# Kernel tuning notes

Measured on AMD Instinct MI355X. Metric: run time of the kernel, lower is better.

The kernel has to match this reference:

```python
import jax, jax.numpy as jnp
import numpy as np
from jax import lax

B, T, F0 = 16, 1024, 128
L_CNN, L_RNN, D = 3, 3, 512
NF = F0 // 2  # 64, freq dim after stride-2 conv
EPS = 1e-5


def conv2d(x, w, b, stride, pad):
    # x: [B,C,H,W], w: [O,I,kh,kw]
    y = lax.conv_general_dilated(x, w, (stride, stride), [(pad, pad), (pad, pad)],
                                 dimension_numbers=('NCHW', 'OIHW', 'NCHW'))
    return y + b[None, :, None, None]


def ln_last(x, g, b):
    m = x.mean(-1, keepdims=True)
    v = ((x - m) ** 2).mean(-1, keepdims=True)
    return (x - m) * lax.rsqrt(v + EPS) * g + b


def ln_feats(x, g, b):
    # LayerNorm over freq axis (axis 2) of [B,C,F,T] (== transpose(2,3); LN; transpose back)
    m = x.mean(2, keepdims=True)
    v = ((x - m) ** 2).mean(2, keepdims=True)
    return (x - m) * lax.rsqrt(v + EPS) * g[None, None, :, None] + b[None, None, :, None]


def sru_dir(u, x_res, v, b, reverse):
    # u: [T,B,3,D] (candidate, f-pre, r-pre); x_res: [T,B,D] highway input; v,b: [2,D]
    u0 = u[:, :, 0]
    fp = u[:, :, 1] + b[0]
    rp = u[:, :, 2] + b[1]

    def step(c, inp):
        u0t, fpt, rpt, xrt = inp
        f = jax.nn.sigmoid(fpt + v[0] * c)
        r = jax.nn.sigmoid(rpt + v[1] * c)
        c = f * c + (1.0 - f) * u0t
        h = r * jnp.tanh(c) + (1.0 - r) * xrt
        return c, h

    c0 = jnp.zeros(u0.shape[1:], u.dtype)
    _, h = lax.scan(step, c0, (u0, fp, rp, x_res), reverse=reverse)
    return h  # [T,B,D]


def _forward(x, cnn_w, cnn_b, res_w1, res_b1, res_w2, res_b2,
             res_ln1_g, res_ln1_b, res_ln2_g, res_ln2_b,
             proj_w, sru_w, sru_v, sru_b, sru_ln_g, sru_ln_b,
             cls_ln_g, cls_ln_b, cls_w1, cls_b1, cls_w2, cls_b2):
    # stem conv: [B,1,128,1024] -> [B,32,64,512]
    x = conv2d(x, cnn_w, cnn_b, 2, 1)
    # residual CNN blocks (dropout = identity in eval)
    for i in range(L_CNN):
        res = x
        h = jax.nn.relu(ln_feats(x, res_ln1_g[i], res_ln1_b[i]))
        h = conv2d(h, res_w1[i], res_b1[i], 1, 1)
        h = jax.nn.relu(ln_feats(h, res_ln2_g[i], res_ln2_b[i]))
        h = conv2d(h, res_w2[i], res_b2[i], 1, 1)
        x = h + res
    # flatten channels x freq, time-major: [T', B, 32*NF]
    b_, c_, f_, t_ = x.shape
    x = x.reshape(b_, c_ * f_, t_).transpose(2, 0, 1)
    # proj_input_to_hidden_first: 2048 -> 2*D
    x = jnp.einsum('tbi,ih->tbh', x, proj_w)
    # bidirectional SRU layers
    for l in range(L_RNN):
        xl = ln_last(x, sru_ln_g[l], sru_ln_b[l])
        # u: [T,B,dir,gate,D]
        u = jnp.einsum('tbi,idkh->tbdkh', xl, sru_w[l])
        h_f = sru_dir(u[:, :, 0], x[..., :D], sru_v[l, 0], sru_b[l, 0], False)
        h_b = sru_dir(u[:, :, 1], x[..., D:], sru_v[l, 1], sru_b[l, 1], True)
        x = jnp.concatenate([h_f, h_b], axis=-1)
    # classifier: [B, T', 2D] -> [B, T', n_vocab+1]
    x = x.transpose(1, 0, 2)
    x = ln_last(x, cls_ln_g, cls_ln_b)
    x = jax.nn.relu(jnp.einsum('bth,hd->btd', x, cls_w1) + cls_b1)
    x = jnp.einsum('btd,dv->btv', x, cls_w2) + cls_b2
    return x


def setup_inputs() -> dict:
    key = jax.random.key(0)
    ks = iter(jax.random.split(key, 40))

    def rn(shape, s=0.05):
        return jax.random.normal(next(ks), shape, jnp.float32) * s

    return dict(
        x=jax.random.normal(next(ks), (B, 1, F0, T), jnp.float32),
        cnn_w=rn((32, 1, 3, 3)), cnn_b=jnp.zeros(32, jnp.float32),
        res_w1=rn((L_CNN, 32, 32, 3, 3)), res_b1=jnp.zeros((L_CNN, 32), jnp.float32),
        res_w2=rn((L_CNN, 32, 32, 3, 3)), res_b2=jnp.zeros((L_CNN, 32), jnp.float32),
        res_ln1_g=jnp.ones((L_CNN, NF), jnp.float32), res_ln1_b=jnp.zeros((L_CNN, NF), jnp.float32),
        res_ln2_g=jnp.ones((L_CNN, NF), jnp.float32), res_ln2_b=jnp.zeros((L_CNN, NF), jnp.float32),
        proj_w=rn((NF * 32, 2 * D), 0.02),
        sru_w=rn((L_RNN, 2 * D, 2, 3, D), 0.02),
        sru_v=rn((L_RNN, 2, 2, D), 0.1),
        sru_b=jnp.zeros((L_RNN, 2, 2, D), jnp.float32),
        sru_ln_g=jnp.ones((L_RNN, 2 * D), jnp.float32), sru_ln_b=jnp.zeros((L_RNN, 2 * D), jnp.float32),
        cls_ln_g=jnp.ones(2 * D, jnp.float32), cls_ln_b=jnp.zeros(2 * D, jnp.float32),
        cls_w1=rn((2 * D, D), 0.02), cls_b1=jnp.zeros(D, jnp.float32),
        cls_w2=rn((D, 29), 0.02), cls_b2=jnp.zeros(29, jnp.float32),
    )


def reference(x, cnn_w, cnn_b, res_w1, res_b1, res_w2, res_b2,
              res_ln1_g, res_ln1_b, res_ln2_g, res_ln2_b,
              proj_w, sru_w, sru_v, sru_b, sru_ln_g, sru_ln_b,
              cls_ln_g, cls_ln_b, cls_w1, cls_b1, cls_w2, cls_b2):
    return _forward(x, cnn_w, cnn_b, res_w1, res_b1, res_w2, res_b2,
                    res_ln1_g, res_ln1_b, res_ln2_g, res_ln2_b,
                    proj_w, sru_w, sru_v, sru_b, sru_ln_g, sru_ln_b,
                    cls_ln_g, cls_ln_b, cls_w1, cls_b1, cls_w2, cls_b2)
```

## Files before the change

kernel.cpp:

```cpp
#include <hip/hip_runtime.h>

typedef unsigned short u16;
typedef unsigned int u32;
typedef __attribute__((ext_vector_type(8))) short short8;
typedef __attribute__((ext_vector_type(4))) float floatx4;

__device__ __forceinline__ float bf2f(u16 u) {
    union { unsigned int i; float f; } v; v.i = ((unsigned int)u) << 16; return v.f;
}
__device__ __forceinline__ u16 f2bf(float f) {
    union { float f; unsigned int i; } v; v.f = f;
    unsigned int i = v.i + 0x7fffu + ((v.i >> 16) & 1u);
    return (u16)(i >> 16);
}

#define GLL(g, l) __builtin_amdgcn_global_load_lds( \
    (const __attribute__((address_space(1))) void*)(g), \
    (__attribute__((address_space(3))) void*)(l), 16, 0, 0)

#define WAITVM(n) asm volatile("s_waitcnt vmcnt(" #n ")" ::: "memory")
#define WAITLG() asm volatile("s_waitcnt lgkmcnt(0)" ::: "memory")
#define SBAR() __builtin_amdgcn_sched_barrier(0)

#define HA_BSTRIDE 1085568

__global__ __launch_bounds__(256) void sniff_k(const u16* __restrict__ x, int* __restrict__ flag) {
    __shared__ int red[4];
    int cnt = 0;
    for (int i = 0; i < 16; ++i) {
        u16 v = x[(threadIdx.x * 16 + i) * 2];
        int e = (v >> 7) & 0xFF;
        if (e >= 110 && e <= 135) cnt++;
    }
    #pragma unroll
    for (int off = 32; off; off >>= 1) cnt += __shfl_down(cnt, off);
    if ((threadIdx.x & 63) == 0) red[threadIdx.x >> 6] = cnt;
    __syncthreads();
    if (threadIdx.x == 0) {
        int tot = red[0] + red[1] + red[2] + red[3];
        *flag = (tot < 2048) ? 1 : 0;
    }
}

__device__ __forceinline__ float ldin(const void* p, size_t i, int isf32) {
    return isf32 ? ((const float*)p)[i] : bf2f(((const u16*)p)[i]);
}

struct CvtArgs {
    const void* src[19];
    int len[19];
    int off[19];
};
__global__ __launch_bounds__(256) void cvtall_k(CvtArgs a, float* __restrict__ dst,
                                                const int* __restrict__ flag) {
    int isf32 = *flag;
    int seg = blockIdx.y;
    int n = a.len[seg];
    const void* s = a.src[seg];
    float* d = dst + a.off[seg];
    for (int i = blockIdx.x * 256 + threadIdx.x; i < n; i += gridDim.x * 256)
        d[i] = ldin(s, i, isf32);
}

__global__ __launch_bounds__(256) void wtr_k(const void* __restrict__ W, int ldw, size_t wofs,
                                             u16* __restrict__ Wt, int ldt,
                                             const int* __restrict__ flag) {
    int isf32 = *flag;
    __shared__ u16 t[64][65];
    int k0 = blockIdx.x * 64, n0 = blockIdx.y * 64;
    int tid = threadIdx.x;
    #pragma unroll
    for (int i = 0; i < 16; ++i) {
        int kk = i * 4 + (tid >> 6), nn = tid & 63;
        t[kk][nn] = f2bf(ldin(W, wofs + (size_t)(k0 + kk) * ldw + n0 + nn, isf32));
    }
    __syncthreads();
    #pragma unroll
    for (int i = 0; i < 16; ++i) {
        int nn = i * 4 + (tid >> 6), kk = tid & 63;
        Wt[(size_t)(n0 + nn) * ldt + k0 + kk] = t[kk][nn];
    }
}

__global__ __launch_bounds__(256) void zero_k(float4* __restrict__ p, int n4) {
    float4 z = {0.f, 0.f, 0.f, 0.f};
    for (int i = blockIdx.x * 256 + threadIdx.x; i < n4; i += gridDim.x * 256) p[i] = z;
}
__global__ __launch_bounds__(256) void fill_k(float* __restrict__ p, int n) {
    int i = blockIdx.x * 256 + threadIdx.x;
    if (i < n) p[i] = 1.0e6f;
}

__global__ __launch_bounds__(256) void conv1_k(const void* __restrict__ x, const float* __restrict__ w,
                                               const float* __restrict__ bias, float* __restrict__ out,
                                               const int* __restrict__ flag) {
    int isf32 = *flag;
    int idx = blockIdx.x * 256 + threadIdx.x;
    int t  = idx & 511;
    int f  = (idx >> 9) & 63;
    int cg = (idx >> 15) & 7;
    int b  = idx >> 18;
    size_t xb = (size_t)b * 128 * 1024;

    float wr[4][9];
    #pragma unroll
    for (int i = 0; i < 4; ++i)
        #pragma unroll
        for (int k = 0; k < 9; ++k) wr[i][k] = w[(cg * 4 + i) * 9 + k];

    float acc[4];
    #pragma unroll
    for (int i = 0; i < 4; ++i) acc[i] = bias[cg * 4 + i];

    #pragma unroll
    for (int df = 0; df < 3; ++df) {
        int fi = 2 * f + df - 1;
        if (fi < 0 || fi >= 128) continue;
        size_t rowb = xb + (size_t)fi * 1024;
        float xv[3];
        #pragma unroll
        for (int dt = 0; dt < 3; ++dt) {
            int ti = 2 * t + dt - 1;
            float v = 0.f;
            if (ti >= 0 && ti < 1024) v = ldin(x, rowb + ti, isf32);
            xv[dt] = v;
        }
        #pragma unroll
        for (int i = 0; i < 4; ++i)
            #pragma unroll
            for (int dt = 0; dt < 3; ++dt)
                acc[i] = fmaf(wr[i][df * 3 + dt], xv[dt], acc[i]);
    }
    size_t obase = (((size_t)b * 32 + cg * 4) * 64 + f) * 512 + t;
    #pragma unroll
    for (int i = 0; i < 4; ++i) out[obase + (size_t)i * 64 * 512] = acc[i];
}

__global__ __launch_bounds__(256) void stats_k(const void* __restrict__ X, int isbf,
                                               float* __restrict__ sm, float* __restrict__ sr) {
    int idx = blockIdx.x * 256 + threadIdx.x;
    int t  = idx & 511;
    int bc = idx >> 9;
    size_t base = (size_t)bc * 64 * 512 + t;
    float s = 0.f, s2 = 0.f;
    #pragma unroll 8
    for (int f = 0; f < 64; ++f) {
        float v = isbf ? bf2f(((const u16*)X)[base + f * 512]) : ((const float*)X)[base + f * 512];
        s += v; s2 += v * v;
    }
    sm[idx] = s;
    sr[idx] = s2;
}

__global__ __launch_bounds__(256) void apply_k(const void* __restrict__ in, int isbf,
                                               const float* __restrict__ sm, const float* __restrict__ sr,
                                               const float* __restrict__ g, const float* __restrict__ be,
                                               u16* __restrict__ Ha) {
    int f = blockIdx.x;
    int b = blockIdx.y;
    float gg = g[f], bb_ = be[f];
    for (int it = 0; it < 2; ++it) {
        int t = it * 256 + threadIdx.x;
        u32 pk[16];
        #pragma unroll
        for (int cp = 0; cp < 16; ++cp) {
            u32 w = 0;
            #pragma unroll
            for (int half = 0; half < 2; ++half) {
                int ci = cp * 2 + half;
                size_t xi = (((size_t)b * 32 + ci) * 64 + f) * 512 + t;
                float xv = isbf ? bf2f(((const u16*)in)[xi]) : ((const float*)in)[xi];
                int si = (b * 32 + ci) * 512 + t;
                float s = sm[si], s2 = sr[si];
                float m = s * (1.f / 64.f);
                float var = fmaxf(s2 * (1.f / 64.f) - m * m, 0.f);
                float rs = rsqrtf(var + 1e-5f);
                float hv = fmaxf((xv - m) * rs * gg + bb_, 0.f);
                w |= ((u32)f2bf(hv)) << (half * 16);
            }
            pk[cp] = w;
        }
        u32* orow = (u32*)(Ha + (size_t)b * HA_BSTRIDE + ((size_t)(f + 1) * 514 + (t + 1)) * 32);
        #pragma unroll
        for (int q = 0; q < 16; ++q) orow[q] = pk[q];
    }
}

#define CVL 4
__global__ __launch_bounds__(256) void convm_k(const u16* __restrict__ Ha, void* __restrict__ out,
                                               const float* __restrict__ w, const float* __restrict__ bias,
                                               const float* __restrict__ res,
                                               float* __restrict__ smx, float* __restrict__ srx) {
    __shared__ __align__(16) u16 act[2][1536 * 8];
    __shared__ float ssS[4][32][17];
    __shared__ float ssQ[4][32][17];
    int F0    = blockIdx.x * 16;
    int tbase = blockIdx.y * 64;
    int b     = blockIdx.z;
    const u16* Hb = Ha + (size_t)b * HA_BSTRIDE;
    int tid  = threadIdx.x;
    int lane = tid & 63;
    int wv   = tid >> 6;
    int quad = lane >> 4;
    int r    = lane & 15;
    int hasres  = (res != nullptr);
    int dostats = (smx != nullptr);

    int ufp[6], utp[6], uq[6];
    #pragma unroll
    for (int it = 0; it < 6; ++it) {
        int u = it * 256 + tid;
        int u2 = (u < 1296) ? u : (u - 1296);
        int fp = u2 / 72;
        int rem = u2 - fp * 72;
        ufp[it] = fp; utp[it] = rem >> 2; uq[it] = rem & 3;
    }

    auto stage = [&](int tile, int bw) {
        int t00 = tbase + tile * 16;
        #pragma unroll
        for (int it = 0; it < 6; ++it) {
            int u = it * 256 + tid;
            GLL(Hb + ((size_t)(F0 + ufp[it]) * 514 + (t00 + utp[it])) * 32 + uq[it] * 8,
                &act[bw][u * 8]);
        }
    };

    short8 bfrag[3][3][2];
    #pragma unroll
    for (int df = 0; df < 3; ++df)
        #pragma unroll
        for (int dt = 0; dt < 3; ++dt)
            #pragma unroll
            for (int ct = 0; ct < 2; ++ct) {
                short8 v;
                #pragma unroll
                for (int j = 0; j < 8; ++j) {
                    int co = ct * 16 + r, ci = quad * 8 + j;
                    v[j] = (short)f2bf(w[(co * 32 + ci) * 9 + df * 3 + dt]);
                }
                bfrag[df][dt][ct] = v;
            }

    WAITVM(0);
    SBAR();
    stage(0, 0);
    SBAR();

    int fb = wv * 4;
    #pragma unroll 1
    for (int i = 0; i < CVL; ++i) {
        if (i < CVL - 1) stage(i + 1, (i + 1) & 1);
        SBAR();
        if (i == 0)           { WAITVM(6); }
        else if (i < CVL - 1) {
            if (hasres) { if (dostats) WAITVM(26); else WAITVM(22); }
            else        { if (dostats) WAITVM(18); else WAITVM(14); }
        } else {
            if (hasres) { if (dostats) WAITVM(20); else WAITVM(16); }
            else        { if (dostats) WAITVM(12); else WAITVM(8); }
        }
        SBAR();
        __builtin_amdgcn_s_barrier();
        SBAR();

        const u16* ab = act[i & 1];
        floatx4 acc[4][2];
        #pragma unroll
        for (int ii = 0; ii < 4; ++ii)
            #pragma unroll
            for (int j = 0; j < 2; ++j)
                #pragma unroll
                for (int k = 0; k < 4; ++k) acc[ii][j][k] = 0.f;

        #pragma unroll
        for (int fh = 0; fh < 6; ++fh) {
            short8 af[3];
            #pragma unroll
            for (int dt = 0; dt < 3; ++dt)
                af[dt] = *(const short8*)&ab[((fb + fh) * 18 + (r + dt)) * 32 + quad * 8];
            #pragma unroll
            for (int df = 0; df < 3; ++df) {
                int rel = fh - df;
                if (rel < 0 || rel >= 4) continue;
                #pragma unroll
                for (int dt = 0; dt < 3; ++dt)
                    #pragma unroll
                    for (int ct = 0; ct < 2; ++ct)
                        acc[rel][ct] = __builtin_amdgcn_mfma_f32_16x16x32_bf16(
                            af[dt], bfrag[df][dt][ct], acc[rel][ct], 0, 0, 0);
            }
        }

        int t0 = tbase + i * 16;
        int tt = t0 + quad * 4;
        float ps[2][4], p2s[2][4];
        #pragma unroll
        for (int ct = 0; ct < 2; ++ct)
            #pragma unroll
            for (int rg = 0; rg < 4; ++rg) { ps[ct][rg] = 0.f; p2s[ct][rg] = 0.f; }

        #pragma unroll
        for (int rel = 0; rel < 4; ++rel)
            #pragma unroll
            for (int ct = 0; ct < 2; ++ct) {
                int f  = F0 + fb + rel;
                int co = ct * 16 + r;
                size_t base = (((size_t)b * 32 + co) * 64 + f) * 512 + tt;
                float bs = bias[co];
                float v4[4];
                if (hasres) {
                    float4 rv = *(const float4*)(res + base);
                    v4[0] = acc[rel][ct][0] + bs + rv.x;
                    v4[1] = acc[rel][ct][1] + bs + rv.y;
                    v4[2] = acc[rel][ct][2] + bs + rv.z;
                    v4[3] = acc[rel][ct][3] + bs + rv.w;
                    float4 o = {v4[0], v4[1], v4[2], v4[3]};
                    *(float4*)((float*)out + base) = o;
                } else {
                    v4[0] = acc[rel][ct][0] + bs;
                    v4[1] = acc[rel][ct][1] + bs;
                    v4[2] = acc[rel][ct][2] + bs;
                    v4[3] = acc[rel][ct][3] + bs;
                    ushort4 o;
                    o.x = f2bf(v4[0]); o.y = f2bf(v4[1]);
                    o.z = f2bf(v4[2]); o.w = f2bf(v4[3]);
                    *(ushort4*)((u16*)out + base) = o;
                }
                #pragma unroll
                for (int rg = 0; rg < 4; ++rg) {
                    ps[ct][rg]  += v4[rg];
                    p2s[ct][rg] += v4[rg] * v4[rg];
                }
            }

        if (dostats) {
            #pragma unroll
            for (int ct = 0; ct < 2; ++ct)
                #pragma unroll
                for (int rg = 0; rg < 4; ++rg) {
                    int co = ct * 16 + r;
                    int j  = quad * 4 + rg;
                    ssS[wv][co][j] = ps[ct][rg];
                    ssQ[wv][co][j] = p2s[ct][rg];
                }
            WAITLG();
            SBAR();
            __builtin_amdgcn_s_barrier();
            SBAR();
            #pragma unroll
            for (int s_ = 0; s_ < 2; ++s_) {
                int slot = s_ * 256 + tid;
                int co = slot >> 4, j = slot & 15;
                float a = ssS[0][co][j] + ssS[1][co][j] + ssS[2][co][j] + ssS[3][co][j];
                float q = ssQ[0][co][j] + ssQ[1][co][j] + ssQ[2][co][j] + ssQ[3][co][j];
                int gi = ((b * 32 + co) << 9) + t0 + j;
                atomicAdd(&smx[gi], a);
                atomicAdd(&srx[gi], q);
            }
        }
        SBAR();
        __builtin_amdgcn_s_barrier();
        SBAR();
    }
}

__global__ __launch_bounds__(256) void transpose_k(const float* __restrict__ X, u16* __restrict__ A) {
    __shared__ float tile[64][65];
    int t0 = blockIdx.x * 64;
    int c  = blockIdx.y;
    int b  = blockIdx.z;
    const float* p = X + (((size_t)b * 32 + c) * 64) * 512 + t0;
    #pragma unroll
    for (int i = 0; i < 16; ++i) {
        int f = i * 4 + (threadIdx.x >> 6);
        int t = threadIdx.x & 63;
        tile[f][t] = p[(size_t)f * 512 + t];
    }
    __syncthreads();
    #pragma unroll
    for (int i = 0; i < 16; ++i) {
        int t = i * 4 + (threadIdx.x >> 6);
        int f = threadIdx.x & 63;
        A[((size_t)(t0 + t) * 16 + b) * 2048 + c * 64 + f] = f2bf(tile[f][t]);
    }
}

__global__ __launch_bounds__(256) void lnlast_k(const float* __restrict__ X, u16* __restrict__ Y,
                                                const float* __restrict__ g, const float* __restrict__ bt,
                                                int width) {
    int row = blockIdx.x;
    int tid = threadIdx.x;
    const float* p = X + (size_t)row * width;
    float4 v4 = *(const float4*)(p + tid * 4);
    float s  = v4.x + v4.y + v4.z + v4.w;
    float s2 = v4.x * v4.x + v4.y * v4.y + v4.z * v4.z + v4.w * v4.w;
    #pragma unroll
    for (int off = 32; off; off >>= 1) { s += __shfl_down(s, off); s2 += __shfl_down(s2, off); }
    __shared__ float red[4][2];
    int wv = tid >> 6;
    if ((tid & 63) == 0) { red[wv][0] = s; red[wv][1] = s2; }
    __syncthreads();
    if (tid == 0) {
        float a = 0.f, b2 = 0.f;
        for (int i = 0; i < 4; ++i) { a += red[i][0]; b2 += red[i][1]; }
        float m = a / width;
        float var = fmaxf(b2 / width - m * m, 0.f);
        red[0][0] = m; red[0][1] = rsqrtf(var + 1e-5f);
    }
    __syncthreads();
    float m = red[0][0], rs = red[0][1];
    float4 g4 = *(const float4*)(g + tid * 4);
    float4 b4 = *(const float4*)(bt + tid * 4);
    ushort4 o;
    o.x = f2bf((v4.x - m) * rs * g4.x + b4.x);
    o.y = f2bf((v4.y - m) * rs * g4.y + b4.y);
    o.z = f2bf((v4.z - m) * rs * g4.z + b4.z);
    o.w = f2bf((v4.w - m) * rs * g4.w + b4.w);
    *(ushort4*)(Y + (size_t)row * width + tid * 4) = o;
}

__global__ __launch_bounds__(256) void gemm_bt(const u16* __restrict__ A, const u16* __restrict__ A2,
                                               int lda, const u16* __restrict__ Bt, int ldb,
                                               void* __restrict__ C, void* __restrict__ C2,
                                               int ldc, int nsplit,
                                               const float* __restrict__ bias, int relu, int K,
                                               int obf) {
    __shared__ __align__(16) u16 As[3][128 * 32];
    __shared__ __align__(16) u16 Bs[3][128 * 32];
    int tid  = threadIdx.x;
    int bm   = blockIdx.x * 128;
    int bn   = blockIdx.y * 128;

    const u16* Ab = A;
    void* Cb = C;
    int cn = bn;
    if (bn >= nsplit) { Ab = A2; Cb = C2; cn = bn - nsplit; }

    int lane = tid & 63;
    int wv   = tid >> 6;
    int quad = lane >> 4;
    int r    = lane & 15;
    int wm   = (wv >> 1) * 64;
    int wn   = (wv & 1) * 64;

    floatx4 acc[4][4];
    #pragma unroll
    for (int i = 0; i < 4; ++i)
        #pragma unroll
        for (int j = 0; j < 4; ++j)
            #pragma unroll
            for (int k = 0; k < 4; ++k) acc[i][j][k] = 0.f;

    int row0 = tid >> 2;
    int ks0  = ((tid & 3) ^ ((tid >> 3) & 3)) * 8;
    const u16* Ab1 = Ab + (size_t)(bm + row0) * lda + ks0;
    const u16* Ab2 = Ab + (size_t)(bm + 64 + row0) * lda + ks0;
    const u16* Bb1 = Bt + (size_t)(bn + row0) * ldb + ks0;
    const u16* Bb2 = Bt + (size_t)(bn + 64 + row0) * ldb + ks0;

    auto stage = [&](int ks, int bw) {
        int k0 = ks * 32;
        GLL(Ab1 + k0, &As[bw][tid * 8]);
        GLL(Ab2 + k0, &As[bw][2048 + tid * 8]);
        GLL(Bb1 + k0, &Bs[bw][tid * 8]);
        GLL(Bb2 + k0, &Bs[bw][2048 + tid * 8]);
    };

    int nk = K >> 5;
    WAITVM(0);
    SBAR();
    stage(0, 0); stage(1, 1); stage(2, 2);
    SBAR();

    int col = (quad ^ ((r >> 1) & 3)) * 8;
    int bc = 0;
    #pragma unroll 1
    for (int i = 0; i < nk; ++i) {
        if (i + 2 < nk)       { WAITVM(8); }
        else if (i + 1 < nk)  { WAITVM(4); }
        else                  { WAITVM(0); }
        SBAR();
        __builtin_amdgcn_s_barrier();
        SBAR();

        const u16* as = As[bc];
        const u16* bs = Bs[bc];
        short8 af[4], bf[4];
        #pragma unroll
        for (int mi = 0; mi < 4; ++mi) af[mi] = *(const short8*)&as[(wm + mi * 16 + r) * 32 + col];
        #pragma unroll
        for (int ni = 0; ni < 4; ++ni) bf[ni] = *(const short8*)&bs[(wn + ni * 16 + r) * 32 + col];
        #pragma unroll
        for (int mi = 0; mi < 4; ++mi)
            #pragma unroll
            for (int ni = 0; ni < 4; ++ni)
                acc[mi][ni] = __builtin_amdgcn_mfma_f32_16x16x32_bf16(af[mi], bf[ni], acc[mi][ni], 0, 0, 0);

        SBAR();
        __builtin_amdgcn_s_barrier();
        SBAR();
        if (i + 3 < nk) stage(i + 3, bc);
        bc = (bc == 2) ? 0 : bc + 1;
    }

    #pragma unroll
    for (int mi = 0; mi < 4; ++mi)
        #pragma unroll
        for (int ni = 0; ni < 4; ++ni) {
            int ccol = cn + wn + ni * 16 + r;
            float bsv = bias ? bias[ccol] : 0.f;
            #pragma unroll
            for (int reg = 0; reg < 4; ++reg) {
                int row = bm + wm + mi * 16 + quad * 4 + reg;
                float v = acc[mi][ni][reg] + bsv;
                if (relu) v = fmaxf(v, 0.f);
                if (obf) ((u16*)Cb)[(size_t)row * ldc + ccol] = f2bf(v);
                else     ((float*)Cb)[(size_t)row * ldc + ccol] = v;
            }
        }
}

#define TC 256
__global__ __launch_bounds__(64) void scan_k(const u16* __restrict__ Uf, const u16* __restrict__ Ub,
                                             const float* __restrict__ Xp, float* __restrict__ Xn,
                                             float* __restrict__ cstate, const float* __restrict__ vv,
                                             const float* __restrict__ bb, int t0f, int t0b, int init) {
    __shared__ __align__(16) char lds[4][10240];
    int tid = threadIdx.x;
    int d   = blockIdx.x >> 7;
    int idx = blockIdx.x & 127;
    int b   = idx >> 3;
    int h0  = (idx & 7) * 64;
    int h   = h0 + tid;
    int gid = d * 8192 + idx * 64 + tid;

    float v0 = vv[(d * 2 + 0) * 512 + h];
    float v1 = vv[(d * 2 + 1) * 512 + h];
    float b0 = bb[(d * 2 + 0) * 512 + h];
    float b1 = bb[(d * 2 + 1) * 512 + h];
    const u16* U = d ? Ub : Uf;
    int t0 = d ? t0b : t0f;
    float* ob = Xn + (size_t)b * 1024 + d * 512 + h;
    float cc = init ? 0.f : cstate[gid];
    int tstp = d ? -16384 : 16384;

    const char* gp[10];
    int dlt[10];
    #pragma unroll
    for (int it = 0; it < 10; ++it) {
        int u = it * 64 + tid;
        int s = u / 40;
        int j = u - s * 40;
        int sl0 = d ? (TC - 1 - s) : s;
        if (j < 24) {
            int k = j >> 3, jj = j & 7;
            gp[it] = (const char*)(U + ((size_t)(sl0 * 16 + b) * 1536 + k * 512 + h0 + jj * 8));
            dlt[it] = d ? -786432 : 786432;
        } else {
            gp[it] = (const char*)(Xp + ((size_t)(t0 + sl0) * 16384 + (size_t)b * 1024 + d * 512 + h0 + (j - 24) * 4));
            dlt[it] = d ? -1048576 : 1048576;
        }
    }
    char* lbase = (char*)&lds[0][0] + tid * 16;
    auto stage = [&](int bw) {
        char* lb = lbase + bw * 10240;
        #pragma unroll
        for (int it = 0; it < 10; ++it) {
            GLL(gp[it], lb + it * 1024);
            gp[it] += dlt[it];
        }
    };

    asm volatile("s_waitcnt vmcnt(0)" ::: "memory");
    SBAR();
    stage(0);
    stage(1);
    stage(2);
    SBAR();

    #pragma unroll 1
    for (int tk = 0; tk < 16; ++tk) {
        switch (tk) {
            case 0:  WAITVM(20); break;
            case 1:  WAITVM(36); break;
            case 14: WAITVM(42); break;
            case 15: WAITVM(32); break;
            default: WAITVM(52); break;
        }
        SBAR();
        const char* Bb = (const char*)&lds[0][0] + (size_t)(tk & 3) * 10240;
        float* op = ob + (size_t)(t0 + (d ? (TC - 1 - tk * 16) : tk * 16)) * 16384;
        #pragma unroll
        for (int s = 0; s < 16; ++s) {
            const char* sb = Bb + s * 640;
            float u0 = bf2f(*(const u16*)(sb + tid * 2));
            float fp = bf2f(*(const u16*)(sb + 128 + tid * 2)) + b0;
            float rp = bf2f(*(const u16*)(sb + 256 + tid * 2)) + b1;
            float xr = *(const float*)(sb + 384 + tid * 4);
            float f = 1.f / (1.f + __expf(-(fp + v0 * cc)));
            float r = 1.f / (1.f + __expf(-(rp + v1 * cc)));
            cc = f * cc + (1.f - f) * u0;
            float th = 1.f - 2.f / (__expf(2.f * cc) + 1.f);
            *op = r * th + (1.f - r) * xr;
            op += tstp;
        }
        SBAR();
        if (tk < 13) stage((tk + 3) & 3);
        SBAR();
    }
    cstate[gid] = cc;
}

__global__ __launch_bounds__(256) void cls2_k(const float* __restrict__ FC1, const float* __restrict__ W2,
                                              const float* __restrict__ b2, void* __restrict__ out,
                                              const int* __restrict__ flag) {
    int isf32 = *flag;
    int tid = threadIdx.x;
    int rh = tid >> 7;
    int ks = (tid >> 5) & 3;
    int v  = tid & 31;
    int row = blockIdx.x * 2 + rh;
    const float* p = FC1 + (size_t)row * 512 + ks * 128;
    const float* wp = W2 + (size_t)ks * 128 * 29;
    float acc = 0.f;
    #pragma unroll 4
    for (int k = 0; k < 128; ++k) {
        float wv = (v < 29) ? wp[k * 29 + v] : 0.f;
        acc = fmaf(p[k], wv, acc);
    }
    acc += __shfl_xor(acc, 32);
    __shared__ float red[2][2][32];
    if ((tid & 63) < 32) red[rh][(tid >> 6) & 1][v] = acc;
    __syncthreads();
    if ((tid & 127) < 32 && v < 29) {
        float s = red[rh][0][v] + red[rh][1][v] + b2[v];
        int t = row >> 4, b = row & 15;
        size_t oi = ((size_t)b * 512 + t) * 29 + v;
        if (isf32) ((float*)out)[oi] = s;
        else       ((u16*)out)[oi]   = f2bf(s);
    }
}

extern "C" void kernel_launch(void* const* d_in, const int* in_sizes, int n_in,
                              void* d_out, int out_size, void* d_ws, size_t ws_size,
                              hipStream_t stream) {
    const void* x      = d_in[0];
    const void* proj_w = d_in[11];
    const void* sru_w  = d_in[12];
    const void* cls_w1 = d_in[19];

    float* ws = (float*)d_ws;
    const size_t O_X    = 0;
    const size_t O_C    = 16777216;
    const size_t O_HA   = 25165824;
    const size_t O_SM   = 33850368;
    const size_t O_SR   = 34112512;
    const size_t O_CST  = 34374656;
    const size_t O_PARK = 34391040;
    const size_t O_FLAG = 34483488;
    const size_t TOTAL  = 34483504;
    if (ws_size < TOTAL * sizeof(float)) {
        fill_k<<<(out_size + 255) / 256, 256, 0, stream>>>((float*)d_out, out_size);
        return;
    }

    float* X   = ws + O_X;
    u16*   C   = (u16*)(ws + O_C);
    u16*   HA  = (u16*)(ws + O_HA);
    float* SM  = ws + O_SM;
    float* SR  = ws + O_SR;
    float* CST = ws + O_CST;
    float* PK  = ws + O_PARK;
    int*   FLG = (int*)(ws + O_FLAG);

    u16*   Abf = (u16*)(ws + O_C);
    u16*   BtP = (u16*)(ws + 0);
    float* XP0 = ws + 25165824;
    u16*   XL  = (u16*)(ws + 0);
    float* XP1 = ws + 4194304;
    u16*   Uf  = (u16*)(ws + 12582912);
    u16*   Ub  = (u16*)(ws + 15728640);
    u16*   BtS = (u16*)(ws + 18874368);
    u16*   BtC = (u16*)(ws + O_SM);
    float* FC1 = ws + 12582912;

    float* p_cnn_w = PK + 0;      float* p_cnn_b = PK + 288;
    float* p_rw1   = PK + 320;    float* p_rb1   = PK + 27968;
    float* p_rw2   = PK + 28064;  float* p_rb2   = PK + 55712;
    float* p_l1g   = PK + 55808;  float* p_l1b   = PK + 56000;
    float* p_l2g   = PK + 56192;  float* p_l2b   = PK + 56384;
    float* p_sv    = PK + 56576;  float* p_sb    = PK + 62720;
    float* p_slng  = PK + 68864;  float* p_slnb  = PK + 71936;
    float* p_clng  = PK + 75008;  float* p_clnb  = PK + 76032;
    float* p_cb1   = PK + 77056;  float* p_cw2   = PK + 77568;
    float* p_cb2   = PK + 92416;

    sniff_k<<<1, 256, 0, stream>>>((const u16*)x, FLG);

    CvtArgs ca;
    const int srcidx[19] = {1,2,3,4,5,6,7,8,9,10,13,14,15,16,17,18,20,21,22};
    const int lens[19]   = {288,32,27648,96,27648,96,192,192,192,192,6144,6144,3072,3072,1024,1024,512,14848,29};
    const int offs[19]   = {0,288,320,27968,28064,55712,55808,56000,56192,56384,56576,62720,68864,71936,75008,76032,77056,77568,92416};
    for (int i = 0; i < 19; ++i) { ca.src[i] = d_in[srcidx[i]]; ca.len[i] = lens[i]; ca.off[i] = offs[i]; }
    cvtall_k<<<dim3(108, 19), 256, 0, stream>>>(ca, PK, FLG);

    zero_k<<<2048, 256, 0, stream>>>((float4*)HA, 2171136);
    conv1_k<<<16384, 256, 0, stream>>>(x, p_cnn_w, p_cnn_b, X, FLG);

    stats_k<<<1024, 256, 0, stream>>>(X, 0, SM, SR);
    for (int i = 0; i < 3; ++i) {
        apply_k<<<dim3(64, 16), 256, 0, stream>>>(X, 0, SM, SR, p_l1g + i * 64, p_l1b + i * 64, HA);
        zero_k<<<512, 256, 0, stream>>>((float4*)SM, 131072);
        convm_k<<<dim3(4, 8, 16), 256, 0, stream>>>(HA, C, p_rw1 + i * 9216, p_rb1 + i * 32,
                                                    nullptr, SM, SR);
        apply_k<<<dim3(64, 16), 256, 0, stream>>>(C, 1, SM, SR, p_l2g + i * 64, p_l2b + i * 64, HA);
        if (i < 2) {
            zero_k<<<512, 256, 0, stream>>>((float4*)SM, 131072);
            convm_k<<<dim3(4, 8, 16), 256, 0, stream>>>(HA, X, p_rw2 + i * 9216, p_rb2 + i * 32,
                                                        X, SM, SR);
        } else {
            convm_k<<<dim3(4, 8, 16), 256, 0, stream>>>(HA, X, p_rw2 + i * 9216, p_rb2 + i * 32,
                                                        X, nullptr, nullptr);
        }
    }

    transpose_k<<<dim3(8, 32, 16), 256, 0, stream>>>(X, Abf);
    wtr_k<<<dim3(32, 16), 256, 0, stream>>>(proj_w, 1024, 0, BtP, 2048, FLG);
    gemm_bt<<<dim3(64, 8), 256, 0, stream>>>(Abf, Abf, 2048, BtP, 2048, XP0, XP0, 1024,
                                             1 << 30, nullptr, 0, 2048, 0);

    for (int l = 0; l < 3; ++l)
        wtr_k<<<dim3(16, 48), 256, 0, stream>>>(sru_w, 3072, (size_t)l * 3145728,
                                                BtS + (size_t)l * 3145728, 1024, FLG);
    wtr_k<<<dim3(16, 8), 256, 0, stream>>>(cls_w1, 512, 0, BtC, 1024, FLG);

    float* cur = XP0;
    float* nxt = XP1;
    for (int l = 0; l < 3; ++l) {
        lnlast_k<<<8192, 256, 0, stream>>>(cur, XL, p_slng + l * 1024, p_slnb + l * 1024, 1024);
        const u16* Btl = BtS + (size_t)l * 3145728;
        for (int j = 0; j < 2; ++j) {
            int t0f = j * TC;
            int t0b = (1 - j) * TC;
            gemm_bt<<<dim3(32, 24), 256, 0, stream>>>(XL + (size_t)t0f * 16 * 1024,
                                                      XL + (size_t)t0b * 16 * 1024, 1024,
                                                      Btl, 1024, Uf, Ub, 1536, 1536,
                                                      nullptr, 0, 1024, 1);
            scan_k<<<256, 64, 0, stream>>>(Uf, Ub, cur, nxt, CST,
                                           p_sv + l * 2048, p_sb + l * 2048, t0f, t0b, j == 0);
        }
        float* tmp = cur; cur = nxt; nxt = tmp;
    }

    lnlast_k<<<8192, 256, 0, stream>>>(cur, XL, p_clng, p_clnb, 1024);
    gemm_bt<<<dim3(64, 4), 256, 0, stream>>>(XL, XL, 1024, BtC, 1024, FC1, FC1, 512,
                                             1 << 30, p_cb1, 1, 1024, 0);
    cls2_k<<<4096, 256, 0, stream>>>(FC1, p_cw2, p_cb2, d_out, FLG);
}
```

Baseline: 1.340 ms.

## Store CNN residual stream in bf16 and shrink conv tiles with LDS atomic stats

The residual activation buffer X is now stored as bf16 instead of fp32. This halves the traffic in conv1, stats, apply, convm residual reads and writes, and transpose, and lets transpose skip its conversion. The convm kernel processes half as many time tiles per block (CVL 4 to 2) and the grid is doubled to keep coverage, which gives more blocks in flight. Per-wave stat partials are replaced by a shared LDS array updated with atomics, which shrinks LDS use. The trade-off is lower precision in the residual accumulation across blocks, plus the cost of LDS atomics.

```diff
diff --git a/kernel.cpp b/kernel.cpp
--- a/kernel.cpp
+++ b/kernel.cpp
@@ -92,7 +92,7 @@
 }
 
 __global__ __launch_bounds__(256) void conv1_k(const void* __restrict__ x, const float* __restrict__ w,
-                                               const float* __restrict__ bias, float* __restrict__ out,
+                                               const float* __restrict__ bias, u16* __restrict__ out,
                                                const int* __restrict__ flag) {
     int isf32 = *flag;
     int idx = blockIdx.x * 256 + threadIdx.x;
@@ -133,10 +133,10 @@
     }
     size_t obase = (((size_t)b * 32 + cg * 4) * 64 + f) * 512 + t;
     #pragma unroll
-    for (int i = 0; i < 4; ++i) out[obase + (size_t)i * 64 * 512] = acc[i];
-}
-
-__global__ __launch_bounds__(256) void stats_k(const void* __restrict__ X, int isbf,
+    for (int i = 0; i < 4; ++i) out[obase + (size_t)i * 64 * 512] = f2bf(acc[i]);
+}
+
+__global__ __launch_bounds__(256) void stats_k(const u16* __restrict__ X,
                                                float* __restrict__ sm, float* __restrict__ sr) {
     int idx = blockIdx.x * 256 + threadIdx.x;
     int t  = idx & 511;
@@ -145,14 +145,14 @@
     float s = 0.f, s2 = 0.f;
     #pragma unroll 8
     for (int f = 0; f < 64; ++f) {
-        float v = isbf ? bf2f(((const u16*)X)[base + f * 512]) : ((const float*)X)[base + f * 512];
+        float v = bf2f(X[base + f * 512]);
         s += v; s2 += v * v;
     }
     sm[idx] = s;
     sr[idx] = s2;
 }
 
-__global__ __launch_bounds__(256) void apply_k(const void* __restrict__ in, int isbf,
+__global__ __launch_bounds__(256) void apply_k(const u16* __restrict__ in,
                                                const float* __restrict__ sm, const float* __restrict__ sr,
                                                const float* __restrict__ g, const float* __restrict__ be,
                                                u16* __restrict__ Ha) {
@@ -169,7 +169,7 @@
             for (int half = 0; half < 2; ++half) {
                 int ci = cp * 2 + half;
                 size_t xi = (((size_t)b * 32 + ci) * 64 + f) * 512 + t;
-                float xv = isbf ? bf2f(((const u16*)in)[xi]) : ((const float*)in)[xi];
+                float xv = bf2f(in[xi]);
                 int si = (b * 32 + ci) * 512 + t;
                 float s = sm[si], s2 = sr[si];
                 float m = s * (1.f / 64.f);
@@ -186,16 +186,16 @@
     }
 }
 
-#define CVL 4
-__global__ __launch_bounds__(256) void convm_k(const u16* __restrict__ Ha, void* __restrict__ out,
+#define CVL 2
+__global__ __launch_bounds__(256) void convm_k(const u16* __restrict__ Ha, u16* __restrict__ out,
                                                const float* __restrict__ w, const float* __restrict__ bias,
-                                               const float* __restrict__ res,
+                                               const u16* __restrict__ res,
                                                float* __restrict__ smx, float* __restrict__ srx) {
     __shared__ __align__(16) u16 act[2][1536 * 8];
-    __shared__ float ssS[4][32][17];
-    __shared__ float ssQ[4][32][17];
+    __shared__ float ssS[32][17];
+    __shared__ float ssQ[32][17];
     int F0    = blockIdx.x * 16;
-    int tbase = blockIdx.y * 64;
+    int tbase = blockIdx.y * 32;
     int b     = blockIdx.z;
     const u16* Hb = Ha + (size_t)b * HA_BSTRIDE;
     int tid  = threadIdx.x;
@@ -226,6 +226,16 @@
         }
     };
 
+    if (dostats) {
+        #pragma unroll
+        for (int s_ = 0; s_ < 2; ++s_) {
+            int slot = s_ * 256 + tid;
+            ssS[slot >> 4][slot & 15] = 0.f;
+            ssQ[slot >> 4][slot & 15] = 0.f;
+        }
+        WAITLG();
+    }
+
     short8 bfrag[3][3][2];
     #pragma unroll
     for (int df = 0; df < 3; ++df)
@@ -252,11 +262,8 @@
     for (int i = 0; i < CVL; ++i) {
         if (i < CVL - 1) stage(i + 1, (i + 1) & 1);
         SBAR();
-        if (i == 0)           { WAITVM(6); }
-        else if (i < CVL - 1) {
-            if (hasres) { if (dostats) WAITVM(26); else WAITVM(22); }
-            else        { if (dostats) WAITVM(18); else WAITVM(14); }
-        } else {
+        if (i == 0) { WAITVM(6); }
+        else {
             if (hasres) { if (dostats) WAITVM(20); else WAITVM(16); }
             else        { if (dostats) WAITVM(12); else WAITVM(8); }
         }
@@ -310,23 +317,21 @@
                 float bs = bias[co];
                 float v4[4];
                 if (hasres) {
-                    float4 rv = *(const float4*)(res + base);
-                    v4[0] = acc[rel][ct][0] + bs + rv.x;
-                    v4[1] = acc[rel][ct][1] + bs + rv.y;
-                    v4[2] = acc[rel][ct][2] + bs + rv.z;
-                    v4[3] = acc[rel][ct][3] + bs + rv.w;
-                    float4 o = {v4[0], v4[1], v4[2], v4[3]};
-                    *(float4*)((float*)out + base) = o;
+                    ushort4 rv = *(const ushort4*)(res + base);
+                    v4[0] = acc[rel][ct][0] + bs + bf2f(rv.x);
+                    v4[1] = acc[rel][ct][1] + bs + bf2f(rv.y);
+                    v4[2] = acc[rel][ct][2] + bs + bf2f(rv.z);
+                    v4[3] = acc[rel][ct][3] + bs + bf2f(rv.w);
                 } else {
                     v4[0] = acc[rel][ct][0] + bs;
                     v4[1] = acc[rel][ct][1] + bs;
                     v4[2] = acc[rel][ct][2] + bs;
                     v4[3] = acc[rel][ct][3] + bs;
-                    ushort4 o;
-                    o.x = f2bf(v4[0]); o.y = f2bf(v4[1]);
-                    o.z = f2bf(v4[2]); o.w = f2bf(v4[3]);
-                    *(ushort4*)((u16*)out + base) = o;
                 }
+                ushort4 o;
+                o.x = f2bf(v4[0]); o.y = f2bf(v4[1]);
+                o.z = f2bf(v4[2]); o.w = f2bf(v4[3]);
+                *(ushort4*)(out + base) = o;
                 #pragma unroll
                 for (int rg = 0; rg < 4; ++rg) {
                     ps[ct][rg]  += v4[rg];
@@ -341,8 +346,8 @@
                 for (int rg = 0; rg < 4; ++rg) {
                     int co = ct * 16 + r;
                     int j  = quad * 4 + rg;
-                    ssS[wv][co][j] = ps[ct][rg];
-                    ssQ[wv][co][j] = p2s[ct][rg];
+                    atomicAdd(&ssS[co][j], ps[ct][rg]);
+                    atomicAdd(&ssQ[co][j], p2s[ct][rg]);
                 }
             WAITLG();
             SBAR();
@@ -352,12 +357,15 @@
             for (int s_ = 0; s_ < 2; ++s_) {
                 int slot = s_ * 256 + tid;
                 int co = slot >> 4, j = slot & 15;
-                float a = ssS[0][co][j] + ssS[1][co][j] + ssS[2][co][j] + ssS[3][co][j];
-                float q = ssQ[0][co][j] + ssQ[1][co][j] + ssQ[2][co][j] + ssQ[3][co][j];
+                float a = ssS[co][j];
+                float q = ssQ[co][j];
+                ssS[co][j] = 0.f;
+                ssQ[co][j] = 0.f;
                 int gi = ((b * 32 + co) << 9) + t0 + j;
                 atomicAdd(&smx[gi], a);
                 atomicAdd(&srx[gi], q);
             }
+            WAITLG();
         }
         SBAR();
         __builtin_amdgcn_s_barrier();
@@ -365,12 +373,12 @@
     }
 }
 
-__global__ __launch_bounds__(256) void transpose_k(const float* __restrict__ X, u16* __restrict__ A) {
-    __shared__ float tile[64][65];
+__global__ __launch_bounds__(256) void transpose_k(const u16* __restrict__ X, u16* __restrict__ A) {
+    __shared__ u16 tile[64][65];
     int t0 = blockIdx.x * 64;
     int c  = blockIdx.y;
     int b  = blockIdx.z;
-    const float* p = X + (((size_t)b * 32 + c) * 64) * 512 + t0;
+    const u16* p = X + (((size_t)b * 32 + c) * 64) * 512 + t0;
     #pragma unroll
     for (int i = 0; i < 16; ++i) {
         int f = i * 4 + (threadIdx.x >> 6);
@@ -382,7 +390,7 @@
     for (int i = 0; i < 16; ++i) {
         int t = i * 4 + (threadIdx.x >> 6);
         int f = threadIdx.x & 63;
-        A[((size_t)(t0 + t) * 16 + b) * 2048 + c * 64 + f] = f2bf(tile[f][t]);
+        A[((size_t)(t0 + t) * 16 + b) * 2048 + c * 64 + f] = tile[f][t];
     }
 }
 
@@ -665,7 +673,7 @@
         return;
     }
 
-    float* X   = ws + O_X;
+    u16*   X   = (u16*)(ws + O_X);
     u16*   C   = (u16*)(ws + O_C);
     u16*   HA  = (u16*)(ws + O_HA);
     float* SM  = ws + O_SM;
@@ -708,20 +716,20 @@
     zero_k<<<2048, 256, 0, stream>>>((float4*)HA, 2171136);
     conv1_k<<<16384, 256, 0, stream>>>(x, p_cnn_w, p_cnn_b, X, FLG);
 
-    stats_k<<<1024, 256, 0, stream>>>(X, 0, SM, SR);
+    stats_k<<<1024, 256, 0, stream>>>(X, SM, SR);
     for (int i = 0; i < 3; ++i) {
-        apply_k<<<dim3(64, 16), 256, 0, stream>>>(X, 0, SM, SR, p_l1g + i * 64, p_l1b + i * 64, HA);
+        apply_k<<<dim3(64, 16), 256, 0, stream>>>(X, SM, SR, p_l1g + i * 64, p_l1b + i * 64, HA);
         zero_k<<<512, 256, 0, stream>>>((float4*)SM, 131072);
-        convm_k<<<dim3(4, 8, 16), 256, 0, stream>>>(HA, C, p_rw1 + i * 9216, p_rb1 + i * 32,
-                                                    nullptr, SM, SR);
-        apply_k<<<dim3(64, 16), 256, 0, stream>>>(C, 1, SM, SR, p_l2g + i * 64, p_l2b + i * 64, HA);
+        convm_k<<<dim3(4, 16, 16), 256, 0, stream>>>(HA, C, p_rw1 + i * 9216, p_rb1 + i * 32,
+                                                     nullptr, SM, SR);
+        apply_k<<<dim3(64, 16), 256, 0, stream>>>(C, SM, SR, p_l2g + i * 64, p_l2b + i * 64, HA);
         if (i < 2) {
             zero_k<<<512, 256, 0, stream>>>((float4*)SM, 131072);
-            convm_k<<<dim3(4, 8, 16), 256, 0, stream>>>(HA, X, p_rw2 + i * 9216, p_rb2 + i * 32,
-                                                        X, SM, SR);
+            convm_k<<<dim3(4, 16, 16), 256, 0, stream>>>(HA, X, p_rw2 + i * 9216, p_rb2 + i * 32,
+                                                         X, SM, SR);
         } else {
-            convm_k<<<dim3(4, 8, 16), 256, 0, stream>>>(HA, X, p_rw2 + i * 9216, p_rb2 + i * 32,
-                                                        X, nullptr, nullptr);
+            convm_k<<<dim3(4, 16, 16), 256, 0, stream>>>(HA, X, p_rw2 + i * 9216, p_rb2 + i * 32,
+                                                         X, nullptr, nullptr);
         }
     }
 
```

Result: slower. 1.640 ms (+22.4%).
